# Optimization experiments

Measured on AMD Instinct MI355X. Metric: run time of the kernel, lower is better.

Reference implementation:

```python
import jax, jax.numpy as jnp
import numpy as np

EPSILON = 0.5

def setup_inputs() -> dict:
    key = jax.random.key(0)
    k1, k2, k3 = jax.random.split(key, 3)
    N, F, D = 8192, 128, 64
    X = jax.random.normal(k1, (N, F), dtype=jnp.float32)
    W_r = jax.random.normal(k2, (2 * F, D), dtype=jnp.float32)
    a_r = jax.random.normal(k3, (D,), dtype=jnp.float32)
    return {"X": X, "W_r": W_r, "a_r": a_r}

def reference(X, W_r, a_r):
    # Faithful to: cat(X_i, X_j) @ W_r @ a_r == (X @ W1 @ a_r)[i] + (X @ W2 @ a_r)[j]
    # (standard GAT decomposition -- avoids materializing [N, N, 2F]).
    F_ = X.shape[1]
    w1 = W_r[:F_] @ a_r          # [F]
    w2 = W_r[F_:] @ a_r          # [F]
    s1 = X @ w1                  # [N]
    s2 = X @ w2                  # [N]
    R = jax.nn.leaky_relu(s1[:, None] + s2[None, :])   # [N, N]
    # torch .std() is unbiased (ddof=1) over all elements
    R = (R - R.mean()) / (jnp.std(R, ddof=1) + 1e-5)
    E = jax.nn.softmax(R, axis=1)
    threshold = E.mean() / EPSILON
    filtered_E = jnp.where(E >= threshold, jnp.float32(1.0), jnp.float32(0.0))
    return filtered_E
```

## Files before the change

### kernel.cpp

```cpp
#include <hip/hip_runtime.h>
#include <math.h>

#define Nn 8192

static constexpr int S1o = 256;
static constexpr int S2o = S1o + Nn;
static constexpr int Mo  = S2o + Nn;
static constexpr int Zo  = Mo + Nn;
static constexpr int RRo = Zo + Nn;
static constexpr int STo = RRo + Nn;

typedef float nfloat4 __attribute__((ext_vector_type(4)));

__device__ __forceinline__ float lrelu32(float z) {
    return (z >= 0.0f) ? z : __fmul_rn(0.01f, z);
}

__device__ __forceinline__ double exp_fast(double x) {
    x = fmin(fmax(x, -700.0), 700.0);
    const double INVLN2 = 1.44269504088896338700e+00;
    const double LN2HI  = 6.93147180369123816490e-01;
    const double LN2LO  = 1.90821492927058770002e-10;
    double nd = rint(x * INVLN2);
    double r  = fma(-nd, LN2HI, x);
    r = fma(-nd, LN2LO, r);
    double p = 1.56192069685862264622e-10;
    p = fma(p, r, 2.08767569878680989792e-09);
    p = fma(p, r, 2.50521083854417187751e-08);
    p = fma(p, r, 2.75573192239858906526e-07);
    p = fma(p, r, 2.75573192239858925110e-06);
    p = fma(p, r, 2.48015873015873015873e-05);
    p = fma(p, r, 1.98412698412698412698e-04);
    p = fma(p, r, 1.38888888888888894069e-03);
    p = fma(p, r, 8.33333333333333321769e-03);
    p = fma(p, r, 4.16666666666666643537e-02);
    p = fma(p, r, 1.66666666666666657415e-01);
    p = fma(p, r, 5.00000000000000000000e-01);
    p = fma(p, r, 1.0);
    p = fma(p, r, 1.0);
    long long n = (long long)nd;
    double sc = __longlong_as_double((n + 1023LL) << 52);
    return p * sc;
}
__device__ __forceinline__ float exp32cr(float x) {
    return (float)exp_fast((double)x);
}

__device__ float blas_dot(const float* __restrict__ a, const float* __restrict__ x, int n) {
    float lane[8];
#pragma unroll
    for (int l = 0; l < 8; ++l) lane[l] = 0.0f;
    for (int k = 0; k < n; k += 8) {
#pragma unroll
        for (int l = 0; l < 8; ++l) lane[l] = __fmaf_rn(a[k + l], x[k + l], lane[l]);
    }
    float s0 = __fadd_rn(lane[0], lane[4]);
    float s1 = __fadd_rn(lane[1], lane[5]);
    float s2 = __fadd_rn(lane[2], lane[6]);
    float s3 = __fadd_rn(lane[3], lane[7]);
    return __fadd_rn(__fadd_rn(s0, s1), __fadd_rn(s2, s3));
}

__device__ __forceinline__ unsigned f2key(float f) {
    unsigned u = __float_as_uint(f);
    return (u & 0x80000000u) ? ~u : (u | 0x80000000u);
}
__device__ __forceinline__ float key2f(unsigned k) {
    unsigned u = (k & 0x80000000u) ? (k & 0x7FFFFFFFu) : ~k;
    return __uint_as_float(u);
}

#define ROW_REDUCE_TAIL_SHFL(RESULT_STMT)                                     \
    {                                                                         \
        __syncthreads();                                                      \
        if (t < 64) {                                                         \
            float sl = __fadd_rn(__fadd_rn(red[t * 8 + 0], red[t * 8 + 1]),   \
                                 __fadd_rn(red[t * 8 + 2], red[t * 8 + 3]));  \
            float sr = __fadd_rn(__fadd_rn(red[t * 8 + 4], red[t * 8 + 5]),   \
                                 __fadd_rn(red[t * 8 + 6], red[t * 8 + 7]));  \
            float v = __fadd_rn(sl, sr);                                      \
            _Pragma("unroll") for (int s_ = 32; s_ >= 1; s_ >>= 1) {          \
                float a_ = __shfl(v, (2 * t) & 63);                           \
                float b_ = __shfl(v, (2 * t + 1) & 63);                       \
                if (t < s_) v = __fadd_rn(a_, b_);                            \
            }                                                                 \
            if (t == 0) { float total = v; RESULT_STMT; }                     \
        }                                                                     \
        __syncthreads();                                                      \
    }

__global__ __launch_bounds__(256) void k_s(const float* __restrict__ X,
                                           const float* __restrict__ Wr,
                                           const float* __restrict__ ar,
                                           float* __restrict__ scr) {
    __shared__ float w1[128], w2[128];
    int t = threadIdx.x;
    if (t < 128) {
        w1[t] = blas_dot(Wr + t * 64, ar, 64);
        w2[t] = blas_dot(Wr + (128 + t) * 64, ar, 64);
    }
    __syncthreads();
    int i = blockIdx.x * 256 + t;
    scr[S1o + i] = blas_dot(X + i * 128, w1, 128);
    scr[S2o + i] = blas_dot(X + i * 128, w2, 128);
}

template <int MODE>
__global__ __launch_bounds__(512) void k_rows_stat16(const float* __restrict__ scr,
                                                     float* __restrict__ rowred) {
    __shared__ float red[512];
    int r0 = blockIdx.x * 16, t = threadIdx.x;
    int l = t >> 3, c = t & 7;
    const float* s2 = scr + S2o;
    int ebase = l * 128 + c;
    float sv[16];
#pragma unroll
    for (int k = 0; k < 16; ++k) sv[k] = s2[ebase + 8 * k];
    float mu = (MODE == 1) ? scr[STo] : 0.0f;
    for (int rr = 0; rr < 16; ++rr) {
        float s1i = scr[S1o + r0 + rr];
        float r;
        if (MODE == 0) {
            r = lrelu32(__fadd_rn(s1i, sv[0]));
#pragma unroll
            for (int k = 1; k < 16; ++k)
                r = __fadd_rn(r, lrelu32(__fadd_rn(s1i, sv[k])));
        } else {
            float d0 = __fsub_rn(lrelu32(__fadd_rn(s1i, sv[0])), mu);
            r = __fmul_rn(d0, d0);
#pragma unroll
            for (int k = 1; k < 16; ++k) {
                float d = __fsub_rn(lrelu32(__fadd_rn(s1i, sv[k])), mu);
                r = __fadd_rn(r, __fmul_rn(d, d));
            }
        }
        red[t] = r;
        ROW_REDUCE_TAIL_SHFL(rowred[r0 + rr] = total)
    }
}

template <int MODE>
__global__ __launch_bounds__(1024) void k_tree(const float* __restrict__ rowred,
                                               float* __restrict__ scr) {
    __shared__ float A[8192];
    __shared__ float B[4096];
    int t = threadIdx.x;
    for (int idx = t; idx < 8192; idx += 1024) A[idx] = rowred[idx];
    __syncthreads();
    float* src = A;
    float* dst = B;
    for (int s = 4096; s >= 1; s >>= 1) {
        for (int idx = t; idx < s; idx += 1024)
            dst[idx] = __fadd_rn(src[2 * idx], src[2 * idx + 1]);
        __syncthreads();
        float* tmp = src; src = dst; dst = tmp;
    }
    if (t == 0) {
        float total = src[0];
        if (MODE == 0) {
            scr[STo] = __fdiv_rn(total, 67108864.0f);
        } else if (MODE == 1) {
            float var = __fdiv_rn(total, 67108864.0f);
            scr[STo + 1] = __fadd_rn(__fsqrt_rn(var), 1e-5f);
        } else {
            float mean = __fdiv_rn(total, 67108864.0f);
            scr[STo + 2] = __fdiv_rn(mean, 0.5f);
        }
    }
}

__global__ __launch_bounds__(512) void k_MZE2(float* __restrict__ scr,
                                              float* __restrict__ rowred) {
    __shared__ float red[512];
    __shared__ float wmax[8];
    __shared__ float Zsh;
    int t = threadIdx.x;
    int l = t >> 3, c = t & 7;
    const float* s2 = scr + S2o;
    float mu = scr[STo], sig = scr[STo + 1];
    int ebase = l * 128 + c;
    float sv[16];
#pragma unroll
    for (int k = 0; k < 16; ++k) sv[k] = s2[ebase + 8 * k];

    for (int rr = 0; rr < 2; ++rr) {
        int i = blockIdx.x * 2 + rr;
        float s1i = scr[S1o + i];

        float rn[16];
        float mx = -3.4e38f;
#pragma unroll
        for (int k = 0; k < 16; ++k) {
            float Rn = __fdiv_rn(__fsub_rn(lrelu32(__fadd_rn(s1i, sv[k])), mu), sig);
            rn[k] = Rn;
            mx = fmaxf(mx, Rn);
        }
#pragma unroll
        for (int o = 32; o > 0; o >>= 1) mx = fmaxf(mx, __shfl_xor(mx, o));
        if ((t & 63) == 0) wmax[t >> 6] = mx;
        __syncthreads();
        float Mi = fmaxf(fmaxf(fmaxf(wmax[0], wmax[1]), fmaxf(wmax[2], wmax[3])),
                         fmaxf(fmaxf(wmax[4], wmax[5]), fmaxf(wmax[6], wmax[7])));

        float p[16];
        p[0] = exp32cr(__fsub_rn(rn[0], Mi));
        float r = p[0];
#pragma unroll
        for (int k = 1; k < 16; ++k) {
            p[k] = exp32cr(__fsub_rn(rn[k], Mi));
            r = __fadd_rn(r, p[k]);
        }
        red[t] = r;
        ROW_REDUCE_TAIL_SHFL(Zsh = total; scr[Zo + i] = total; scr[Mo + i] = Mi)
        float Zi = Zsh;

        float e = __fdiv_rn(p[0], Zi);
#pragma unroll
        for (int k = 1; k < 16; ++k)
            e = __fadd_rn(e, __fdiv_rn(p[k], Zi));
        red[t] = e;
        ROW_REDUCE_TAIL_SHFL(rowred[i] = total)
    }
}

__global__ __launch_bounds__(256) void k_out(const float* __restrict__ scr,
                                             float* __restrict__ out) {
    __shared__ unsigned kcut[8][3];
    int t = threadIdx.x;
    int r0 = blockIdx.x * 8;
    float mu = scr[STo], sig = scr[STo + 1], thr = scr[STo + 2];
    if (t < 24) {
        int rr = t / 3, w = t - rr * 3;
        int i = r0 + rr;
        float s1i = scr[S1o + i];
        float Mi = scr[Mo + i], Zi = scr[Zo + i];
        double thr_d = (double)thr;
        unsigned lo = 0x00800000u;
        unsigned hi = 0xFF800000u;
        while (lo < hi) {
            unsigned mid = lo + ((hi - lo) >> 1);
            float s2v = key2f(mid);
            float Rn = __fdiv_rn(__fsub_rn(lrelu32(__fadd_rn(s1i, s2v)), mu), sig);
            float P = exp32cr(__fsub_rn(Rn, Mi));
            float E = __fdiv_rn(P, Zi);
            double m = ((double)E - thr_d) / thr_d;
            bool pred = (w == 0) ? (m >= -2.8e-8)
                      : (w == 1) ? (m > 2.8e-8)
                                 : (m >= 1.75e-7);
            if (pred) hi = mid; else lo = mid + 1;
        }
        kcut[rr][w] = lo;
    }
    __syncthreads();
    unsigned kA[8], kB[8], kC[8];
    long long rowbase[8];
#pragma unroll
    for (int rr = 0; rr < 8; ++rr) {
        kA[rr] = kcut[rr][0];
        kB[rr] = kcut[rr][1];
        kC[rr] = kcut[rr][2];
        rowbase[rr] = (long long)(r0 + rr) * Nn;
    }
    const float* s2 = scr + S2o;
    for (int ch = 0; ch < 8; ++ch) {
        int j0 = ch * 1024 + t * 4;
        nfloat4 sv = *reinterpret_cast<const nfloat4*>(s2 + j0);
        unsigned k0 = f2key(sv.x), k1 = f2key(sv.y), k2 = f2key(sv.z), k3 = f2key(sv.w);
#pragma unroll
        for (int rr = 0; rr < 8; ++rr) {
            unsigned a = kA[rr], b = kB[rr], cc = kC[rr];
            nfloat4 r;
            r.x = (k0 < a) ? 0.0f : (k0 < b) ? 1.0f : (k0 < cc) ? 0.0f : 1.0f;
            r.y = (k1 < a) ? 0.0f : (k1 < b) ? 1.0f : (k1 < cc) ? 0.0f : 1.0f;
            r.z = (k2 < a) ? 0.0f : (k2 < b) ? 1.0f : (k2 < cc) ? 0.0f : 1.0f;
            r.w = (k3 < a) ? 0.0f : (k3 < b) ? 1.0f : (k3 < cc) ? 0.0f : 1.0f;
            __builtin_nontemporal_store(r, reinterpret_cast<nfloat4*>(out + rowbase[rr] + j0));
        }
    }
}

extern "C" void kernel_launch(void* const* d_in, const int* in_sizes, int n_in,
                              void* d_out, int out_size, void* d_ws, size_t ws_size,
                              hipStream_t stream) {
    const float *X = nullptr, *Wr = nullptr, *ar = nullptr;
    for (int k = 0; k < n_in; ++k) {
        if      (in_sizes[k] == 1048576) X  = (const float*)d_in[k];
        else if (in_sizes[k] == 16384)   Wr = (const float*)d_in[k];
        else if (in_sizes[k] == 64)      ar = (const float*)d_in[k];
    }
    if (!X)  X  = (const float*)d_in[0];
    if (!Wr) Wr = (const float*)d_in[1];
    if (!ar) ar = (const float*)d_in[2];

    float* out = (float*)d_out;
    float* scr = (float*)d_ws;
    float* rowred = scr + RRo;

    k_s             <<<32,   256, 0, stream>>>(X, Wr, ar, scr);
    k_rows_stat16<0><<<512,  512, 0, stream>>>(scr, rowred);
    k_tree<0>       <<<1,   1024, 0, stream>>>(rowred, scr);
    k_rows_stat16<1><<<512,  512, 0, stream>>>(scr, rowred);
    k_tree<1>       <<<1,   1024, 0, stream>>>(rowred, scr);
    k_MZE2          <<<4096, 512, 0, stream>>>(scr, rowred);
    k_tree<2>       <<<1,   1024, 0, stream>>>(rowred, scr);
    k_out           <<<1024, 256, 0, stream>>>(scr, out);
}
```

Baseline: 207.9 us.

## Fuse global tree reductions into consumer kernels to drop launches

Removes two single-block tree-reduction kernels by having every block of the next kernel (k_stat1 and k_out) redundantly reload the 8192 row partials and run the same bitwise-identical pairwise tree in shared memory. This saves kernel launches and serial single-block phases in exchange for extra redundant shared-memory work and 32 KB of LDS per block, which may lower occupancy. A separate buffer is added for the variance partials so the mean partials are not overwritten while other blocks still read them.

```diff
diff --git a/kernel.cpp b/kernel.cpp
--- a/kernel.cpp
+++ b/kernel.cpp
@@ -9,6 +9,7 @@
 static constexpr int Zo  = Mo + Nn;
 static constexpr int RRo = Zo + Nn;
 static constexpr int STo = RRo + Nn;
+static constexpr int RBo = STo + 8;
 
 typedef float nfloat4 __attribute__((ext_vector_type(4)));
 
@@ -89,6 +90,22 @@
         __syncthreads();                                                      \
     }
 
+#define GLOBAL_TREE_INPLACE(Abuf, NT, TOTALVAR)                               \
+    {                                                                         \
+        for (int s_ = 4096; s_ >= 1; s_ >>= 1) {                              \
+            float v_[16];                                                     \
+            int n_ = 0;                                                       \
+            for (int idx = t; idx < s_; idx += NT)                            \
+                v_[n_++] = __fadd_rn(Abuf[2 * idx], Abuf[2 * idx + 1]);       \
+            __syncthreads();                                                  \
+            n_ = 0;                                                           \
+            for (int idx = t; idx < s_; idx += NT)                            \
+                Abuf[idx] = v_[n_++];                                         \
+            __syncthreads();                                                  \
+        }                                                                     \
+        TOTALVAR = Abuf[0];                                                   \
+    }
+
 __global__ __launch_bounds__(256) void k_s(const float* __restrict__ X,
                                            const float* __restrict__ Wr,
                                            const float* __restrict__ ar,
@@ -105,9 +122,8 @@
     scr[S2o + i] = blas_dot(X + i * 128, w2, 128);
 }
 
-template <int MODE>
-__global__ __launch_bounds__(512) void k_rows_stat16(const float* __restrict__ scr,
-                                                     float* __restrict__ rowred) {
+__global__ __launch_bounds__(512) void k_stat0(const float* __restrict__ scr,
+                                               float* __restrict__ rowredA) {
     __shared__ float red[512];
     int r0 = blockIdx.x * 16, t = threadIdx.x;
     int l = t >> 3, c = t & 7;
@@ -116,36 +132,56 @@
     float sv[16];
 #pragma unroll
     for (int k = 0; k < 16; ++k) sv[k] = s2[ebase + 8 * k];
-    float mu = (MODE == 1) ? scr[STo] : 0.0f;
     for (int rr = 0; rr < 16; ++rr) {
         float s1i = scr[S1o + r0 + rr];
-        float r;
-        if (MODE == 0) {
-            r = lrelu32(__fadd_rn(s1i, sv[0]));
-#pragma unroll
-            for (int k = 1; k < 16; ++k)
-                r = __fadd_rn(r, lrelu32(__fadd_rn(s1i, sv[k])));
-        } else {
-            float d0 = __fsub_rn(lrelu32(__fadd_rn(s1i, sv[0])), mu);
-            r = __fmul_rn(d0, d0);
-#pragma unroll
-            for (int k = 1; k < 16; ++k) {
-                float d = __fsub_rn(lrelu32(__fadd_rn(s1i, sv[k])), mu);
-                r = __fadd_rn(r, __fmul_rn(d, d));
-            }
-        }
+        float r = lrelu32(__fadd_rn(s1i, sv[0]));
+#pragma unroll
+        for (int k = 1; k < 16; ++k)
+            r = __fadd_rn(r, lrelu32(__fadd_rn(s1i, sv[k])));
         red[t] = r;
-        ROW_REDUCE_TAIL_SHFL(rowred[r0 + rr] = total)
-    }
-}
-
-template <int MODE>
-__global__ __launch_bounds__(1024) void k_tree(const float* __restrict__ rowred,
-                                               float* __restrict__ scr) {
+        ROW_REDUCE_TAIL_SHFL(rowredA[r0 + rr] = total)
+    }
+}
+
+__global__ __launch_bounds__(512) void k_stat1(float* __restrict__ scr) {
+    __shared__ float A[8192];
+    __shared__ float red[512];
+    int r0 = blockIdx.x * 16, t = threadIdx.x;
+    const float* rowredA = scr + RRo;
+    float* rowredB = scr + RBo;
+    for (int idx = t; idx < 8192; idx += 512) A[idx] = rowredA[idx];
+    __syncthreads();
+    float total;
+    GLOBAL_TREE_INPLACE(A, 512, total)
+    float mu = __fdiv_rn(total, 67108864.0f);
+    if (blockIdx.x == 0 && t == 0) scr[STo] = mu;
+
+    int l = t >> 3, c = t & 7;
+    const float* s2 = scr + S2o;
+    int ebase = l * 128 + c;
+    float sv[16];
+#pragma unroll
+    for (int k = 0; k < 16; ++k) sv[k] = s2[ebase + 8 * k];
+    for (int rr = 0; rr < 16; ++rr) {
+        float s1i = scr[S1o + r0 + rr];
+        float d0 = __fsub_rn(lrelu32(__fadd_rn(s1i, sv[0])), mu);
+        float r = __fmul_rn(d0, d0);
+#pragma unroll
+        for (int k = 1; k < 16; ++k) {
+            float d = __fsub_rn(lrelu32(__fadd_rn(s1i, sv[k])), mu);
+            r = __fadd_rn(r, __fmul_rn(d, d));
+        }
+        red[t] = r;
+        ROW_REDUCE_TAIL_SHFL(rowredB[r0 + rr] = total)
+    }
+}
+
+__global__ __launch_bounds__(1024) void k_tree_sig(const float* __restrict__ rowredB,
+                                                   float* __restrict__ scr) {
     __shared__ float A[8192];
     __shared__ float B[4096];
     int t = threadIdx.x;
-    for (int idx = t; idx < 8192; idx += 1024) A[idx] = rowred[idx];
+    for (int idx = t; idx < 8192; idx += 1024) A[idx] = rowredB[idx];
     __syncthreads();
     float* src = A;
     float* dst = B;
@@ -156,24 +192,16 @@
         float* tmp = src; src = dst; dst = tmp;
     }
     if (t == 0) {
-        float total = src[0];
-        if (MODE == 0) {
-            scr[STo] = __fdiv_rn(total, 67108864.0f);
-        } else if (MODE == 1) {
-            float var = __fdiv_rn(total, 67108864.0f);
-            scr[STo + 1] = __fadd_rn(__fsqrt_rn(var), 1e-5f);
-        } else {
-            float mean = __fdiv_rn(total, 67108864.0f);
-            scr[STo + 2] = __fdiv_rn(mean, 0.5f);
-        }
-    }
-}
-
-__global__ __launch_bounds__(512) void k_MZE2(float* __restrict__ scr,
-                                              float* __restrict__ rowred) {
+        float var = __fdiv_rn(src[0], 67108864.0f);
+        scr[STo + 1] = __fadd_rn(__fsqrt_rn(var), 1e-5f);
+    }
+}
+
+__global__ __launch_bounds__(512) void k_MZE2(float* __restrict__ scr) {
     __shared__ float red[512];
     __shared__ float wmax[8];
     __shared__ float Zsh;
+    float* rowredE = scr + RRo;
     int t = threadIdx.x;
     int l = t >> 3, c = t & 7;
     const float* s2 = scr + S2o;
@@ -187,13 +215,12 @@
         int i = blockIdx.x * 2 + rr;
         float s1i = scr[S1o + i];
 
-        float rn[16];
+        float v[16];
         float mx = -3.4e38f;
 #pragma unroll
         for (int k = 0; k < 16; ++k) {
-            float Rn = __fdiv_rn(__fsub_rn(lrelu32(__fadd_rn(s1i, sv[k])), mu), sig);
-            rn[k] = Rn;
-            mx = fmaxf(mx, Rn);
+            v[k] = __fdiv_rn(__fsub_rn(lrelu32(__fadd_rn(s1i, sv[k])), mu), sig);
+            mx = fmaxf(mx, v[k]);
         }
 #pragma unroll
         for (int o = 32; o > 0; o >>= 1) mx = fmaxf(mx, __shfl_xor(mx, o));
@@ -202,33 +229,41 @@
         float Mi = fmaxf(fmaxf(fmaxf(wmax[0], wmax[1]), fmaxf(wmax[2], wmax[3])),
                          fmaxf(fmaxf(wmax[4], wmax[5]), fmaxf(wmax[6], wmax[7])));
 
-        float p[16];
-        p[0] = exp32cr(__fsub_rn(rn[0], Mi));
-        float r = p[0];
+        v[0] = exp32cr(__fsub_rn(v[0], Mi));
+        float r = v[0];
 #pragma unroll
         for (int k = 1; k < 16; ++k) {
-            p[k] = exp32cr(__fsub_rn(rn[k], Mi));
-            r = __fadd_rn(r, p[k]);
+            v[k] = exp32cr(__fsub_rn(v[k], Mi));
+            r = __fadd_rn(r, v[k]);
         }
         red[t] = r;
         ROW_REDUCE_TAIL_SHFL(Zsh = total; scr[Zo + i] = total; scr[Mo + i] = Mi)
         float Zi = Zsh;
 
-        float e = __fdiv_rn(p[0], Zi);
+        float e = __fdiv_rn(v[0], Zi);
 #pragma unroll
         for (int k = 1; k < 16; ++k)
-            e = __fadd_rn(e, __fdiv_rn(p[k], Zi));
+            e = __fadd_rn(e, __fdiv_rn(v[k], Zi));
         red[t] = e;
-        ROW_REDUCE_TAIL_SHFL(rowred[i] = total)
+        ROW_REDUCE_TAIL_SHFL(rowredE[i] = total)
     }
 }
 
 __global__ __launch_bounds__(256) void k_out(const float* __restrict__ scr,
                                              float* __restrict__ out) {
+    __shared__ float A[8192];
     __shared__ unsigned kcut[8][3];
     int t = threadIdx.x;
     int r0 = blockIdx.x * 8;
-    float mu = scr[STo], sig = scr[STo + 1], thr = scr[STo + 2];
+    const float* rowredE = scr + RRo;
+    for (int idx = t; idx < 8192; idx += 256) A[idx] = rowredE[idx];
+    __syncthreads();
+    float total;
+    GLOBAL_TREE_INPLACE(A, 256, total)
+    float mean = __fdiv_rn(total, 67108864.0f);
+    float thr = __fdiv_rn(mean, 0.5f);
+    float mu = scr[STo], sig = scr[STo + 1];
+
     if (t < 24) {
         int rr = t / 3, w = t - rr * 3;
         int i = r0 + rr;
@@ -294,14 +329,11 @@
 
     float* out = (float*)d_out;
     float* scr = (float*)d_ws;
-    float* rowred = scr + RRo;
-
-    k_s             <<<32,   256, 0, stream>>>(X, Wr, ar, scr);
-    k_rows_stat16<0><<<512,  512, 0, stream>>>(scr, rowred);
-    k_tree<0>       <<<1,   1024, 0, stream>>>(rowred, scr);
-    k_rows_stat16<1><<<512,  512, 0, stream>>>(scr, rowred);
-    k_tree<1>       <<<1,   1024, 0, stream>>>(rowred, scr);
-    k_MZE2          <<<4096, 512, 0, stream>>>(scr, rowred);
-    k_tree<2>       <<<1,   1024, 0, stream>>>(rowred, scr);
-    k_out           <<<1024, 256, 0, stream>>>(scr, out);
-}
+
+    k_s        <<<32,   256, 0, stream>>>(X, Wr, ar, scr);
+    k_stat0    <<<512,  512, 0, stream>>>(scr, scr + RRo);
+    k_stat1    <<<512,  512, 0, stream>>>(scr);
+    k_tree_sig <<<1,   1024, 0, stream>>>(scr + RBo, scr);
+    k_MZE2     <<<4096, 512, 0, stream>>>(scr);
+    k_out      <<<1024, 256, 0, stream>>>(scr, out);
+}
```

Measured after the change: 209.0 us. Within noise of the previous version (+0.5%).
